# Kernel tuning notes

Hardware: AMD Instinct MI355X
Metric: run time of the kernel (lower is better)

The kernel has to match this reference:

```python
import math
import jax, jax.numpy as jnp
import numpy as np

B, H, W, CV = 8, 64, 64, 256
T, CT = 77, 512
NH, TOP_M = 8, 5
CLAMP = 2.0

def _ln(x, g, b, eps=1e-5):
    mu = x.mean(-1, keepdims=True)
    var = ((x - mu) ** 2).mean(-1, keepdims=True)
    return (x - mu) / jnp.sqrt(var + eps) * g + b

def _l2norm(x, eps=1e-6):
    n = jnp.sqrt((x * x).sum(-1, keepdims=True))
    return x / jnp.maximum(n, eps)

def _xavier(key, fan_in, fan_out):
    a = math.sqrt(6.0 / (fan_in + fan_out))
    return jax.random.uniform(key, (fan_in, fan_out), jnp.float32, -a, a)

def setup_inputs() -> dict:
    key = jax.random.key(0)
    ks = jax.random.split(key, 12)
    inp = {
        'visual_features': jax.random.normal(ks[0], (B, H, W, CV), jnp.float32),
        'text_features': jax.random.normal(ks[1], (B, T, CT), jnp.float32),
        'Wq': _xavier(ks[2], CV, CV), 'bq': jnp.zeros((CV,), jnp.float32),
        'Wk': _xavier(ks[3], CT, CV), 'bk': jnp.zeros((CV,), jnp.float32),
        'Wv': _xavier(ks[4], CT, CV), 'bv': jnp.zeros((CV,), jnp.float32),
        'Wo': _xavier(ks[5], CV, CV), 'bo': jnp.zeros((CV,), jnp.float32),
        'g1': jnp.ones((CV,), jnp.float32), 'b1': jnp.zeros((CV,), jnp.float32),
        'g2': jnp.ones((CV,), jnp.float32), 'b2': jnp.zeros((CV,), jnp.float32),
        'W_ffn1': jax.random.normal(ks[6], (CV, 4 * CV), jnp.float32) * 0.02,
        'b_ffn1': jnp.zeros((4 * CV,), jnp.float32),
        'W_ffn2': jax.random.normal(ks[7], (4 * CV, CV), jnp.float32) * 0.02,
        'b_ffn2': jnp.zeros((CV,), jnp.float32),
        'logit_scale': jnp.float32(math.log(1.0 / 0.07)),
        'alpha': jnp.float32(0.1),
    }
    return inp

def _topm_mask(sim, m):
    # keep only top-m entries along last axis (scatter of top-k indices)
    t = sim.shape[-1]
    _, topi = jax.lax.top_k(sim, m)
    keep = jax.vmap(lambda idx: jnp.zeros((t,), bool).at[idx].set(True))(
        topi.reshape(-1, m)).reshape(sim.shape)
    return jnp.where(keep, sim, -jnp.inf)

def _forward(visual_features, text_features, Wq, bq, Wk, bk, Wv, bv, Wo, bo,
             g1, b1, g2, b2, W_ffn1, b_ffn1, W_ffn2, b_ffn2, logit_scale, alpha):
    b, h, w, cv = visual_features.shape
    n = h * w
    dh = cv // NH
    x = _ln(visual_features, g1, b1).reshape(b, n, cv)      # Pre-LN, (B,N,Cv)
    q = (x @ Wq + bq).reshape(b, n, NH, dh)
    k = (text_features @ Wk + bk).reshape(b, T, NH, dh)
    v = (text_features @ Wv + bv).reshape(b, T, NH, dh)
    q = _l2norm(q); k = _l2norm(k)                           # cosine attention
    scale = jnp.exp(jnp.clip(logit_scale, -CLAMP, CLAMP)) / jnp.sqrt(jnp.float32(dh))
    sim = jnp.einsum('bnhd,bthd->bnht', q, k) * scale        # (B,N,H,T)
    pad = jnp.abs(text_features).sum(-1) <= 1e-6             # (B,T) pad tokens
    sim = jnp.where(pad[:, None, None, :], -jnp.inf, sim)
    sim = _topm_mask(sim, TOP_M)
    attn = jax.nn.softmax(sim, axis=-1)
    all_pad = pad.all(axis=1)                                # (B,)
    attn = jnp.where(all_pad[:, None, None, None], 0.0, attn)
    aligned = jnp.einsum('bnht,bthd->bnhd', attn, v).reshape(b, n, cv)
    aligned = aligned @ Wo + bo
    y = x + alpha * aligned
    y = _ln(y, g2, b2)
    hdn = jax.nn.gelu(y @ W_ffn1 + b_ffn1, approximate=False)
    y = y + (hdn @ W_ffn2 + b_ffn2)
    return y.reshape(b, h, w, cv)

def reference(visual_features, text_features, Wq, bq, Wk, bk, Wv, bv, Wo, bo,
              g1, b1, g2, b2, W_ffn1, b_ffn1, W_ffn2, b_ffn2, logit_scale, alpha):
    return _forward(visual_features, text_features, Wq, bq, Wk, bk, Wv, bv, Wo, bo,
                    g1, b1, g2, b2, W_ffn1, b_ffn1, W_ffn2, b_ffn2, logit_scale, alpha)
```

## Files before the change

kernel.cpp:

```cpp
#include <hip/hip_runtime.h>
#include <math.h>

#define NB   8
#define NPIX 4096
#define MROW 32768
#define CV_  256
#define TT   77
#define CT_  512
#define NH_  8
#define DH_  32
#define BT_  616

typedef __bf16 bf16x8 __attribute__((ext_vector_type(8)));
typedef float  f32x4  __attribute__((ext_vector_type(4)));

__device__ __forceinline__ float bf2f(unsigned short u) {
  return __uint_as_float(((unsigned)u) << 16);
}
__device__ __forceinline__ unsigned short f2b(float f) {
  unsigned u = __float_as_uint(f);
  return (unsigned short)((u + 0x7FFFu + ((u >> 16) & 1u)) >> 16);
}
__device__ __forceinline__ unsigned pack2(float lo, float hi) {
  return ((unsigned)f2b(hi) << 16) | (unsigned)f2b(lo);
}
__device__ __forceinline__ void async_copy16(const unsigned short* g,
                                             unsigned short* l) {
  __builtin_amdgcn_global_load_lds(
      (const __attribute__((address_space(1))) void*)g,
      (__attribute__((address_space(3))) void*)l, 16, 0, 0);
}
__device__ __forceinline__ float gelu_t(float v) {
  float p = v * fmaf(0.0713548162726f, v * v, 1.59576912161f);
  float e = __expf(p);
  return v - v / (e + 1.0f);
}

__global__ __launch_bounds__(256) void prep_kernel(
    const float* __restrict__ visual, const float* __restrict__ g1,
    const float* __restrict__ b1, unsigned short* __restrict__ xbuf,
    const float* __restrict__ s0, const float* __restrict__ s1,
    const float* __restrict__ s2, const float* __restrict__ s3,
    const float* __restrict__ s4, const float* __restrict__ s5,
    unsigned short* __restrict__ d0, unsigned short* __restrict__ d1,
    unsigned short* __restrict__ d2, unsigned short* __restrict__ d3,
    unsigned short* __restrict__ d4, unsigned short* __restrict__ d5,
    const float* __restrict__ bk, const float* __restrict__ bv,
    float* __restrict__ bkv, const float* __restrict__ text,
    float* __restrict__ padb) {
  int bx = blockIdx.x;
  int wave = threadIdx.x >> 6, lane = threadIdx.x & 63;
  if (bx < 8192) {
    int row = bx * 4 + wave;
    size_t base = (size_t)row * 256 + lane * 4;
    float4 f = *reinterpret_cast<const float4*>(visual + base);
    float v0 = f.x, v1 = f.y, v2 = f.z, v3 = f.w;
    float s = v0 + v1 + v2 + v3;
    float q = v0 * v0 + v1 * v1 + v2 * v2 + v3 * v3;
#pragma unroll
    for (int off = 1; off < 64; off <<= 1) {
      s += __shfl_xor(s, off);
      q += __shfl_xor(q, off);
    }
    float mean = s * (1.0f / 256.0f);
    float var  = q * (1.0f / 256.0f) - mean * mean;
    float rstd = rsqrtf(var + 1e-5f);
    float4 gv = *reinterpret_cast<const float4*>(g1 + lane * 4);
    float4 bv4 = *reinterpret_cast<const float4*>(b1 + lane * 4);
    ushort4 o;
    o.x = f2b((v0 - mean) * rstd * gv.x + bv4.x);
    o.y = f2b((v1 - mean) * rstd * gv.y + bv4.y);
    o.z = f2b((v2 - mean) * rstd * gv.z + bv4.z);
    o.w = f2b((v3 - mean) * rstd * gv.w + bv4.w);
    *reinterpret_cast<ushort4*>(xbuf + base) = o;
    return;
  }
  if (bx >= 11778) {
    int row = (bx - 11778) * 4 + wave;
    const float* tr = text + (size_t)row * CT_ + lane * 8;
    float4 f0 = *reinterpret_cast<const float4*>(tr);
    float4 f1 = *reinterpret_cast<const float4*>(tr + 4);
    float s = fabsf(f0.x) + fabsf(f0.y) + fabsf(f0.z) + fabsf(f0.w)
            + fabsf(f1.x) + fabsf(f1.y) + fabsf(f1.z) + fabsf(f1.w);
#pragma unroll
    for (int off = 1; off < 64; off <<= 1) s += __shfl_xor(s, off);
    if (lane == 0) padb[row] = (s <= 1e-6f) ? 1.0f : 0.0f;
    return;
  }
  int gi = (bx - 8192) * 256 + threadIdx.x;
  const float* src; unsigned short* dst; int R, C, idx;
  if      (gi < 65536)  { src=s0; dst=d0; R=256;  C=256;  idx=gi; }
  else if (gi < 196608) { src=s1; dst=d1; R=512;  C=256;  idx=gi-65536; }
  else if (gi < 327680) { src=s2; dst=d2; R=512;  C=256;  idx=gi-196608; }
  else if (gi < 393216) { src=s3; dst=d3; R=256;  C=256;  idx=gi-327680; }
  else if (gi < 655360) { src=s4; dst=d4; R=256;  C=1024; idx=gi-393216; }
  else if (gi < 917504) { src=s5; dst=d5; R=1024; C=256;  idx=gi-655360; }
  else if (gi < 918016) {
    int i = gi - 917504;
    bkv[i] = (i < 256) ? bk[i] : bv[i - 256];
    return;
  } else return;
  int r = idx / C, c = idx - r * C;
  dst[(size_t)c * R + r] = f2b(src[idx]);
}

__global__ __launch_bounds__(256) void qkv_kernel(
    const unsigned short* __restrict__ xb, const unsigned short* __restrict__ WqT,
    const float* __restrict__ bq, unsigned short* __restrict__ qout,
    const float* __restrict__ text, const unsigned short* __restrict__ WkvT,
    const float* __restrict__ bkv, float* __restrict__ kout,
    float* __restrict__ vout) {
  __shared__ unsigned short lA[4096];
  __shared__ unsigned short lB[4096];
  int tid = threadIdx.x;
  int lane = tid & 63, wave = tid >> 6;
  int l15 = lane & 15, quad = lane >> 4;
  if (blockIdx.x < 512) {
    int bm = (blockIdx.x >> 1) * 128, bn = (blockIdx.x & 1) * 128;
    int wm = (wave & 1) * 64, wn = (wave >> 1) * 64;
    int crow = lane >> 2, ccol = (lane & 3) * 8;
    f32x4 acc[4][4] = {};
    for (int k0 = 0; k0 < 256; k0 += 32) {
#pragma unroll
      for (int ch = 0; ch < 2; ++ch) {
        int c = wave * 2 + ch;
        async_copy16(xb + (size_t)(bm + c * 16 + crow) * 256 + k0 + ccol,
                     &lA[c * 512]);
        async_copy16(WqT + (size_t)(bn + c * 16 + crow) * 256 + k0 + ccol,
                     &lB[c * 512]);
      }
      __syncthreads();
      bf16x8 af[4], bfr[4];
#pragma unroll
      for (int mi = 0; mi < 4; ++mi)
        af[mi] = *reinterpret_cast<const bf16x8*>(&lA[(wm + mi * 16 + l15) * 32 + quad * 8]);
#pragma unroll
      for (int ni = 0; ni < 4; ++ni)
        bfr[ni] = *reinterpret_cast<const bf16x8*>(&lB[(wn + ni * 16 + l15) * 32 + quad * 8]);
#pragma unroll
      for (int mi = 0; mi < 4; ++mi)
#pragma unroll
        for (int ni = 0; ni < 4; ++ni)
          acc[mi][ni] = __builtin_amdgcn_mfma_f32_16x16x32_bf16(af[mi], bfr[ni],
                                                                acc[mi][ni], 0, 0, 0);
      __syncthreads();
    }
#pragma unroll
    for (int mi = 0; mi < 4; ++mi) {
#pragma unroll
      for (int ni = 0; ni < 4; ++ni) {
        int gcol = bn + wn + ni * 16 + l15;
        float bsf = bq[gcol];
#pragma unroll
        for (int r = 0; r < 4; ++r) {
          int grow = bm + wm + mi * 16 + quad * 4 + r;
          qout[(size_t)grow * 256 + gcol] = f2b(acc[mi][ni][r] + bsf);
        }
      }
    }
  } else {
    int i = blockIdx.x - 512;
    int bm = (i % 10) * 64, bn = (i / 10) * 64;
    int srow = tid >> 2, sc8 = (tid & 3) * 8;
    int wm = (wave & 1) * 32, wn = (wave >> 1) * 32;
    f32x4 acc[2][2] = {};
    int gm = bm + srow, gn = bn + srow;
    const bool aok = (gm < BT_);
    for (int k0 = 0; k0 < CT_; k0 += 32) {
      uint4 apk = make_uint4(0, 0, 0, 0);
      if (aok) {
        const float* Af = text + (size_t)gm * CT_ + k0 + sc8;
        float4 f0 = *reinterpret_cast<const float4*>(Af);
        float4 f1 = *reinterpret_cast<const float4*>(Af + 4);
        apk.x = pack2(f0.x, f0.y); apk.y = pack2(f0.z, f0.w);
        apk.z = pack2(f1.x, f1.y); apk.w = pack2(f1.z, f1.w);
      }
      uint4 bpk = *reinterpret_cast<const uint4*>(WkvT + (size_t)gn * CT_ + k0 + sc8);
      *reinterpret_cast<uint4*>(&lA[srow * 40 + sc8]) = apk;
      *reinterpret_cast<uint4*>(&lB[srow * 40 + sc8]) = bpk;
      __syncthreads();
      bf16x8 a0 = *reinterpret_cast<const bf16x8*>(&lA[(wm + l15) * 40 + quad * 8]);
      bf16x8 a1 = *reinterpret_cast<const bf16x8*>(&lA[(wm + 16 + l15) * 40 + quad * 8]);
      bf16x8 b0 = *reinterpret_cast<const bf16x8*>(&lB[(wn + l15) * 40 + quad * 8]);
      bf16x8 b1 = *reinterpret_cast<const bf16x8*>(&lB[(wn + 16 + l15) * 40 + quad * 8]);
      acc[0][0] = __builtin_amdgcn_mfma_f32_16x16x32_bf16(a0, b0, acc[0][0], 0, 0, 0);
      acc[0][1] = __builtin_amdgcn_mfma_f32_16x16x32_bf16(a0, b1, acc[0][1], 0, 0, 0);
      acc[1][0] = __builtin_amdgcn_mfma_f32_16x16x32_bf16(a1, b0, acc[1][0], 0, 0, 0);
      acc[1][1] = __builtin_amdgcn_mfma_f32_16x16x32_bf16(a1, b1, acc[1][1], 0, 0, 0);
      __syncthreads();
    }
#pragma unroll
    for (int mt = 0; mt < 2; ++mt) {
#pragma unroll
      for (int nt = 0; nt < 2; ++nt) {
        int gcol = bn + wn + nt * 16 + l15;
        float bsf = bkv[gcol];
#pragma unroll
        for (int r = 0; r < 4; ++r) {
          int grow = bm + wm + mt * 16 + quad * 4 + r;
          if (grow >= BT_) continue;
          float v = acc[mt][nt][r] + bsf;
          if (gcol < 256) kout[(size_t)grow * 256 + gcol] = v;
          else            vout[(size_t)grow * 256 + gcol - 256] = v;
        }
      }
    }
  }
}

__global__ __launch_bounds__(256) void gemm_oln(
    const unsigned short* __restrict__ A, const unsigned short* __restrict__ Bt,
    const float* __restrict__ bias, const unsigned short* __restrict__ xres,
    const float* __restrict__ alpha_ptr,
    const float* __restrict__ g2, const float* __restrict__ b2,
    unsigned short* __restrict__ ybf, float* __restrict__ yf32) {
  __shared__ unsigned short sm[16384];
  unsigned short* lA = sm;
  unsigned short* lB = sm + 2048;
  unsigned short* yt = sm;
  const int K = 256;
  int tid = threadIdx.x;
  int bm = blockIdx.x * 64;
  int lane = tid & 63, wave = tid >> 6;
  int wm = (wave & 1) * 32, wn = (wave >> 1) * 128;
  int l15 = lane & 15, quad = lane >> 4;
  int crow = lane >> 2, ccol = (lane & 3) * 8;
  f32x4 acc[2][8] = {};
  for (int k0 = 0; k0 < K; k0 += 32) {
    async_copy16(A + (size_t)(bm + wave * 16 + crow) * K + k0 + ccol,
                 &lA[wave * 512]);
#pragma unroll
    for (int ch = wave; ch < 16; ch += 4)
      async_copy16(Bt + (size_t)(ch * 16 + crow) * K + k0 + ccol,
                   &lB[ch * 512]);
    __syncthreads();
    bf16x8 af[2], bfr[8];
#pragma unroll
    for (int mi = 0; mi < 2; ++mi)
      af[mi] = *reinterpret_cast<const bf16x8*>(&lA[(wm + mi * 16 + l15) * 32 + quad * 8]);
#pragma unroll
    for (int ni = 0; ni < 8; ++ni)
      bfr[ni] = *reinterpret_cast<const bf16x8*>(&lB[(wn + ni * 16 + l15) * 32 + quad * 8]);
#pragma unroll
    for (int mi = 0; mi < 2; ++mi)
#pragma unroll
      for (int ni = 0; ni < 8; ++ni)
        acc[mi][ni] = __builtin_amdgcn_mfma_f32_16x16x32_bf16(af[mi], bfr[ni],
                                                              acc[mi][ni], 0, 0, 0);
    __syncthreads();
  }
  float alpha = *alpha_ptr;
#pragma unroll
  for (int mi = 0; mi < 2; ++mi) {
#pragma unroll
    for (int ni = 0; ni < 8; ++ni) {
      int gcol = wn + ni * 16 + l15;
      float bsf = bias[gcol];
#pragma unroll
      for (int r = 0; r < 4; ++r) {
        int lrow = wm + mi * 16 + quad * 4 + r;
        float v = acc[mi][ni][r] + bsf;
        float y0 = bf2f(xres[(size_t)(bm + lrow) * 256 + gcol]) + alpha * v;
        yt[lrow * 256 + gcol] = f2b(y0);
      }
    }
  }
  __syncthreads();
  for (int it = 0; it < 16; ++it) {
    int row = wave * 16 + it;
    ushort4 u = *reinterpret_cast<const ushort4*>(&yt[row * 256 + lane * 4]);
    float v0 = bf2f(u.x), v1 = bf2f(u.y), v2 = bf2f(u.z), v3 = bf2f(u.w);
    float s = v0 + v1 + v2 + v3;
    float q = v0 * v0 + v1 * v1 + v2 * v2 + v3 * v3;
#pragma unroll
    for (int off = 1; off < 64; off <<= 1) {
      s += __shfl_xor(s, off);
      q += __shfl_xor(q, off);
    }
    float mean = s * (1.0f / 256.0f);
    float var  = q * (1.0f / 256.0f) - mean * mean;
    float rstd = rsqrtf(var + 1e-5f);
    float4 gv = *reinterpret_cast<const float4*>(g2 + lane * 4);
    float4 bv = *reinterpret_cast<const float4*>(b2 + lane * 4);
    float o0 = (v0 - mean) * rstd * gv.x + bv.x;
    float o1 = (v1 - mean) * rstd * gv.y + bv.y;
    float o2 = (v2 - mean) * rstd * gv.z + bv.z;
    float o3 = (v3 - mean) * rstd * gv.w + bv.w;
    size_t base = (size_t)(bm + row) * 256 + lane * 4;
    ushort4 ob;
    ob.x = f2b(o0); ob.y = f2b(o1); ob.z = f2b(o2); ob.w = f2b(o3);
    *reinterpret_cast<ushort4*>(ybf + base) = ob;
    *reinterpret_cast<float4*>(yf32 + base) = make_float4(o0, o1, o2, o3);
  }
}

#define SSTR 83
#define VSTR 33
#define NEGBIG -3.0e38f
__device__ __forceinline__ void ins5(float sv, float& tv0, float& tv1,
                                     float& tv2, float& tv3, float& tv4) {
  bool g0 = sv > tv0, g1 = sv > tv1, g2 = sv > tv2, g3 = sv > tv3, g4 = sv > tv4;
  tv4 = g4 ? (g3 ? tv3 : sv) : tv4;
  tv3 = g3 ? (g2 ? tv2 : sv) : tv3;
  tv2 = g2 ? (g1 ? tv1 : sv) : tv2;
  tv1 = g1 ? (g0 ? tv0 : sv) : tv1;
  tv0 = g0 ? sv : tv0;
}
__global__ __launch_bounds__(256) void attn_kernel(
    unsigned short* qa, const float* __restrict__ k,
    const float* __restrict__ v, const float* __restrict__ padb,
    const float* __restrict__ ls_ptr) {
  __shared__ unsigned short qb[64 * 40];
  __shared__ unsigned short kb[80 * 40];
  __shared__ float S[64 * SSTR];
  __shared__ float vs[TT * VSTR];
  __shared__ float rn[64];
  __shared__ float scs[80];
  __shared__ int allpad_s;
  int tid = threadIdx.x;
  int h = blockIdx.y, b = blockIdx.z;
  size_t qbase = ((size_t)b * NPIX + blockIdx.x * 64) * CV_ + h * DH_;
  size_t kvbase = (size_t)b * TT * CV_ + h * DH_;
  float ls = *ls_ptr;
  ls = fminf(fmaxf(ls, -2.0f), 2.0f);
  float scale = expf(ls) * 0.17677669529663687f;
  if (tid == 0) allpad_s = 1;
  __syncthreads();
  int qrow = tid >> 2, qq = tid & 3;
  uint4 qv4 = *reinterpret_cast<const uint4*>(qa + qbase + (size_t)qrow * CV_ + qq * 8);
  *reinterpret_cast<uint4*>(&qb[qrow * 40 + qq * 8]) = qv4;
  {
    float ssq = 0.f;
    unsigned w[4] = {qv4.x, qv4.y, qv4.z, qv4.w};
#pragma unroll
    for (int i = 0; i < 4; ++i) {
      float a = bf2f((unsigned short)(w[i] & 0xFFFF));
      float bb = bf2f((unsigned short)(w[i] >> 16));
      ssq += a * a + bb * bb;
    }
    ssq += __shfl_xor(ssq, 1);
    ssq += __shfl_xor(ssq, 2);
    if (qq == 0) rn[qrow] = scale / fmaxf(sqrtf(ssq), 1e-6f);
  }
  if (tid < 154) {
    int kr = tid >> 1, kh = tid & 1;
    const float* kp = k + kvbase + (size_t)kr * CV_ + kh * 16;
    float4 f0 = *reinterpret_cast<const float4*>(kp);
    float4 f1 = *reinterpret_cast<const float4*>(kp + 4);
    float4 f2 = *reinterpret_cast<const float4*>(kp + 8);
    float4 f3 = *reinterpret_cast<const float4*>(kp + 12);
    float ks2 = f0.x*f0.x + f0.y*f0.y + f0.z*f0.z + f0.w*f0.w
              + f1.x*f1.x + f1.y*f1.y + f1.z*f1.z + f1.w*f1.w
              + f2.x*f2.x + f2.y*f2.y + f2.z*f2.z + f2.w*f2.w
              + f3.x*f3.x + f3.y*f3.y + f3.z*f3.z + f3.w*f3.w;
    uint4 p0, p1;
    p0.x = pack2(f0.x, f0.y); p0.y = pack2(f0.z, f0.w);
    p0.z = pack2(f1.x, f1.y); p0.w = pack2(f1.z, f1.w);
    p1.x = pack2(f2.x, f2.y); p1.y = pack2(f2.z, f2.w);
    p1.z = pack2(f3.x, f3.y); p1.w = pack2(f3.z, f3.w);
    *reinterpret_cast<uint4*>(&kb[kr * 40 + kh * 16]) = p0;
    *reinterpret_cast<uint4*>(&kb[kr * 40 + kh * 16 + 8]) = p1;
    ks2 += __shfl_xor(ks2, 1);
    if (kh == 0) {
      float p = padb[b * TT + kr];
      float sc = (p == 0.0f) ? 1.0f / fmaxf(sqrtf(ks2), 1e-6f) : 0.0f;
      scs[kr] = sc;
      if (sc > 0.0f) allpad_s = 0;
    }
  } else if (tid < 157) {
    scs[77 + (tid - 154)] = 0.0f;
  } else if (tid >= 160 && tid < 172) {
    int i = tid - 160;
    *reinterpret_cast<uint4*>(&kb[(77 + (i >> 2)) * 40 + (i & 3) * 8]) =
        make_uint4(0, 0, 0, 0);
  }
  for (int j = tid; j < TT * 8; j += 256) {
    int t = j >> 3, d4 = j & 7;
    float4 f = *reinterpret_cast<const float4*>(
        v + kvbase + (size_t)t * CV_ + d4 * 4);
    float* vp = &vs[t * VSTR + d4 * 4];
    vp[0] = f.x; vp[1] = f.y; vp[2] = f.z; vp[3] = f.w;
  }
  __syncthreads();
  {
    int lane = tid & 63, wave = tid >> 6;
    int wm = wave * 16;
    int l15 = lane & 15, quad = lane >> 4;
    f32x4 acc[5] = {};
    bf16x8 af = *reinterpret_cast<const bf16x8*>(&qb[(wm + l15) * 40 + quad * 8]);
    bf16x8 bfr[5];
#pragma unroll
    for (int ni = 0; ni < 5; ++ni)
      bfr[ni] = *reinterpret_cast<const bf16x8*>(&kb[(ni * 16 + l15) * 40 + quad * 8]);
#pragma unroll
    for (int ni = 0; ni < 5; ++ni)
      acc[ni] = __builtin_amdgcn_mfma_f32_16x16x32_bf16(af, bfr[ni], acc[ni], 0, 0, 0);
#pragma unroll
    for (int ni = 0; ni < 5; ++ni) {
      int col = ni * 16 + l15;
      float sc = scs[col];
#pragma unroll
      for (int r = 0; r < 4; ++r) {
        int row = wm + quad * 4 + r;
        float val = (sc > 0.0f) ? acc[ni][r] * rn[row] * sc : NEGBIG;
        unsigned pb = (__float_as_uint(val) & 0xFFFFFF80u) | (unsigned)col;
        S[row * SSTR + col] = __uint_as_float(pb);
      }
    }
  }
  __syncthreads();
  int allpad = allpad_s;
  int row = qrow;
  const float* Srow = &S[row * SSTR];
  int t0 = qq * 20, t1 = (qq == 3) ? TT : t0 + 20;
  float tv0 = -INFINITY, tv1 = -INFINITY, tv2 = -INFINITY,
        tv3 = -INFINITY, tv4 = -INFINITY;
  for (int t = t0; t < t1; ++t)
    ins5(Srow[t], tv0, tv1, tv2, tv3, tv4);
#pragma unroll
  for (int m = 1; m <= 2; m <<= 1) {
    float n0 = __shfl_xor(tv0, m), n1 = __shfl_xor(tv1, m),
          n2 = __shfl_xor(tv2, m), n3 = __shfl_xor(tv3, m),
          n4 = __shfl_xor(tv4, m);
    ins5(n0, tv0, tv1, tv2, tv3, tv4);
    ins5(n1, tv0, tv1, tv2, tv3, tv4);
    ins5(n2, tv0, tv1, tv2, tv3, tv4);
    ins5(n3, tv0, tv1, tv2, tv3, tv4);
    ins5(n4, tv0, tv1, tv2, tv3, tv4);
  }
  float o[8];
#pragma unroll
  for (int d = 0; d < 8; ++d) o[d] = 0.f;
  if (!allpad) {
    float e0 = 1.0f;
    float e1 = expf(tv1 - tv0);
    float e2 = expf(tv2 - tv0);
    float e3 = expf(tv3 - tv0);
    float e4 = expf(tv4 - tv0);
    float inv = 1.0f / (e0 + e1 + e2 + e3 + e4);
    int i0 = __float_as_uint(tv0) & 0x7F, i1 = __float_as_uint(tv1) & 0x7F,
        i2 = __float_as_uint(tv2) & 0x7F, i3 = __float_as_uint(tv3) & 0x7F,
        i4 = __float_as_uint(tv4) & 0x7F;
    const float* v0p = &vs[i0 * VSTR + qq * 8];
    const float* v1p = &vs[i1 * VSTR + qq * 8];
    const float* v2p = &vs[i2 * VSTR + qq * 8];
    const float* v3p = &vs[i3 * VSTR + qq * 8];
    const float* v4p = &vs[i4 * VSTR + qq * 8];
#pragma unroll
    for (int d = 0; d < 8; ++d)
      o[d] = (e0 * v0p[d] + e1 * v1p[d] + e2 * v2p[d] + e3 * v3p[d] + e4 * v4p[d]) * inv;
  }
  unsigned short* qp = qa + qbase + (size_t)row * CV_ + qq * 8;
  uint4 ou;
  ou.x = ((unsigned)f2b(o[1]) << 16) | f2b(o[0]);
  ou.y = ((unsigned)f2b(o[3]) << 16) | f2b(o[2]);
  ou.z = ((unsigned)f2b(o[5]) << 16) | f2b(o[4]);
  ou.w = ((unsigned)f2b(o[7]) << 16) | f2b(o[6]);
  *reinterpret_cast<uint4*>(qp) = ou;
}

#define XSTR 264
#define HSTR 136
__global__ __launch_bounds__(512) void ffn_fused(
    const unsigned short* __restrict__ ybf, const unsigned short* __restrict__ W1T,
    const float* __restrict__ b1f, const unsigned short* __restrict__ W2T,
    const float* __restrict__ b2f, float* __restrict__ yio) {
  __shared__ unsigned short xs[128 * XSTR];
  __shared__ unsigned short Hs[128 * HSTR];
  __shared__ unsigned short Wb[16384];
  int tid = threadIdx.x, lane = tid & 63, wave = tid >> 6;
  int l15 = lane & 15, quad = lane >> 4;
  int crow = lane >> 2;
  int ccs = (((lane & 3) ^ ((lane >> 3) & 3)) * 8);
  int rsw = ((quad ^ ((l15 >> 1) & 3)) * 8);
  int bm = blockIdx.x * 128;
  {
    int row = tid >> 2, kh = (tid & 3) * 64;
    const unsigned short* src = ybf + (size_t)(bm + row) * 256 + kh;
    unsigned short* dst = &xs[row * XSTR + kh];
#pragma unroll
    for (int i = 0; i < 8; ++i)
      *reinterpret_cast<uint4*>(dst + i * 8) =
          *reinterpret_cast<const uint4*>(src + i * 8);
  }
  int wm2 = (wave & 1) * 64, wn2 = (wave >> 1) * 64;
  int wh1 = (wave & 1) * 64, wr1 = (wave >> 1) * 32;
  auto stage = [&](int st) {
    st &= 63;
    int c = st >> 3, p = st & 7;
    unsigned short* buf = &Wb[(st & 1) * 8192];
    if (p < 4) {
#pragma unroll
      for (int sl = 0; sl < 2; ++sl)
        async_copy16(W1T + (size_t)(c * 128 + wave * 16 + crow) * 256
                         + p * 64 + sl * 32 + ccs,
                     &buf[sl * 4096 + wave * 512]);
    } else {
      int q = p - 4;
#pragma unroll
      for (int i = 0; i < 2; ++i)
        async_copy16(W2T + (size_t)((wave * 2 + i) * 16 + crow) * 1024
                         + c * 128 + q * 32 + ccs,
                     &buf[(wave * 2 + i) * 512]);
    }
  };
  f32x4 acc[4][4] = {};
  stage(0); stage(1);
  for (int c = 0; c < 8; ++c) {
    f32x4 acc1[4][2] = {};
#pragma unroll
    for (int p = 0; p < 8; ++p) {
      int st = c * 8 + p;
      asm volatile("s_waitcnt vmcnt(2) lgkmcnt(0)" ::: "memory");
      __builtin_amdgcn_s_barrier();
      __builtin_amdgcn_sched_barrier(0);
      const unsigned short* buf = &Wb[(p & 1) * 8192];
      if (p < 4) {
#pragma unroll
        for (int sl = 0; sl < 2; ++sl) {
          int k = p * 64 + sl * 32;
          bf16x8 af[4], bfr[2];
#pragma unroll
          for (int mi = 0; mi < 4; ++mi)
            af[mi] = *reinterpret_cast<const bf16x8*>(
                &buf[sl * 4096 + (wh1 + mi * 16 + l15) * 32 + rsw]);
#pragma unroll
          for (int ni = 0; ni < 2; ++ni)
            bfr[ni] = *reinterpret_cast<const bf16x8*>(
                &xs[(wr1 + ni * 16 + l15) * XSTR + k + quad * 8]);
          __builtin_amdgcn_s_setprio(1);
#pragma unroll
          for (int mi = 0; mi < 4; ++mi)
#pragma unroll
            for (int ni = 0; ni < 2; ++ni)
              acc1[mi][ni] = __builtin_amdgcn_mfma_f32_16x16x32_bf16(
                  af[mi], bfr[ni], acc1[mi][ni], 0, 0, 0);
          __builtin_amdgcn_s_setprio(0);
        }
        if (p == 3) {
#pragma unroll
          for (int mi = 0; mi < 4; ++mi) {
            int hb = wh1 + mi * 16 + quad * 4;
            float b0 = b1f[c * 128 + hb],      b1v = b1f[c * 128 + hb + 1];
            float b2v = b1f[c * 128 + hb + 2], b3 = b1f[c * 128 + hb + 3];
#pragma unroll
            for (int ni = 0; ni < 2; ++ni) {
              int row = wr1 + ni * 16 + l15;
              ushort4 hw;
              hw.x = f2b(gelu_t(acc1[mi][ni][0] + b0));
              hw.y = f2b(gelu_t(acc1[mi][ni][1] + b1v));
              hw.z = f2b(gelu_t(acc1[mi][ni][2] + b2v));
              hw.w = f2b(gelu_t(acc1[mi][ni][3] + b3));
              *reinterpret_cast<ushort4*>(&Hs[row * HSTR + hb]) = hw;
            }
          }
        }
      } else {
        int q = p - 4, kk = q * 32;
        bf16x8 af[4], bfr[4];
#pragma unroll
        for (int mi = 0; mi < 4; ++mi)
          af[mi] = *reinterpret_cast<const bf16x8*>(
              &Hs[(wm2 + mi * 16 + l15) * HSTR + kk + quad * 8]);
#pragma unroll
        for (int ni = 0; ni < 4; ++ni)
          bfr[ni] = *reinterpret_cast<const bf16x8*>(
              &buf[(wn2 + ni * 16 + l15) * 32 + rsw]);
        __builtin_amdgcn_s_setprio(1);
#pragma unroll
        for (int mi = 0; mi < 4; ++mi)
#pragma unroll
          for (int ni = 0; ni < 4; ++ni)
            acc[mi][ni] = __builtin_amdgcn_mfma_f32_16x16x32_bf16(
                af[mi], bfr[ni], acc[mi][ni], 0, 0, 0);
        __builtin_amdgcn_s_setprio(0);
      }
      __builtin_amdgcn_sched_barrier(0);
      __builtin_amdgcn_s_barrier();
      __builtin_amdgcn_sched_barrier(0);
      stage(st + 2);
    }
  }
  asm volatile("s_waitcnt vmcnt(0)" ::: "memory");
#pragma unroll
  for (int mi = 0; mi < 4; ++mi)
#pragma unroll
    for (int ni = 0; ni < 4; ++ni) {
      int col = wn2 + ni * 16 + l15;
      float bs = b2f[col];
#pragma unroll
      for (int r = 0; r < 4; ++r) {
        int g = bm + wm2 + mi * 16 + quad * 4 + r;
        size_t oi = (size_t)g * 256 + col;
        yio[oi] = yio[oi] + acc[mi][ni][r] + bs;
      }
    }
}

extern "C" void kernel_launch(void* const* d_in, const int* in_sizes, int n_in,
                              void* d_out, int out_size, void* d_ws, size_t ws_size,
                              hipStream_t stream) {
  const float* visual = (const float*)d_in[0];
  const float* text   = (const float*)d_in[1];
  const float* Wq  = (const float*)d_in[2];
  const float* bq  = (const float*)d_in[3];
  const float* Wk  = (const float*)d_in[4];
  const float* bk  = (const float*)d_in[5];
  const float* Wv  = (const float*)d_in[6];
  const float* bv  = (const float*)d_in[7];
  const float* Wo  = (const float*)d_in[8];
  const float* bo  = (const float*)d_in[9];
  const float* g1  = (const float*)d_in[10];
  const float* b1  = (const float*)d_in[11];
  const float* g2  = (const float*)d_in[12];
  const float* b2  = (const float*)d_in[13];
  const float* W1  = (const float*)d_in[14];
  const float* bf1 = (const float*)d_in[15];
  const float* W2  = (const float*)d_in[16];
  const float* bff2 = (const float*)d_in[17];
  const float* lsc = (const float*)d_in[18];
  const float* alp = (const float*)d_in[19];

  char* ws = (char*)d_ws;
  size_t off = 0;
  auto alloc = [&](size_t bytes) -> char* {
    char* p = ws + off;
    off += (bytes + 255) & ~(size_t)255;
    return p;
  };
  unsigned short* WqT = (unsigned short*)alloc((size_t)65536 * 2);
  unsigned short* WkT = (unsigned short*)alloc((size_t)131072 * 2);
  unsigned short* WvT = (unsigned short*)alloc((size_t)131072 * 2);
  unsigned short* WoT = (unsigned short*)alloc((size_t)65536 * 2);
  unsigned short* W1T = (unsigned short*)alloc((size_t)262144 * 2);
  unsigned short* W2T = (unsigned short*)alloc((size_t)262144 * 2);
  float*          bkv  = (float*)alloc(512 * 4);
  float*          kbuf = (float*)alloc((size_t)BT_ * CV_ * 4);
  float*          vbuf = (float*)alloc((size_t)BT_ * CV_ * 4);
  float*          padb = (float*)alloc((size_t)BT_ * 4);
  char* U = ws + off;
  unsigned short* xbuf = (unsigned short*)U;
  unsigned short* qbuf = (unsigned short*)(U + 16777216);
  float*          ybuf = (float*)d_out;

  prep_kernel<<<11932, 256, 0, stream>>>(visual, g1, b1, xbuf,
                                         Wq, Wk, Wv, Wo, W1, W2,
                                         WqT, WkT, WvT, WoT, W1T, W2T,
                                         bk, bv, bkv, text, padb);
  qkv_kernel<<<592, 256, 0, stream>>>(xbuf, WqT, bq, qbuf,
                                      text, WkT, bkv, kbuf, vbuf);
  attn_kernel<<<dim3(64, NH_, NB), 256, 0, stream>>>(qbuf, kbuf, vbuf, padb, lsc);
  gemm_oln<<<512, 256, 0, stream>>>(qbuf, WoT, bo, xbuf, alp, g2, b2,
                                    xbuf, ybuf);
  ffn_fused<<<256, 512, 0, stream>>>(xbuf, W1T, bf1, W2T, bff2, ybuf);
}
```

Measured before the change: 287.2 us.

## Triple-buffer FFN weight stages, drop bf16 y copy, cache bias in LDS

The FFN kernel's weight staging goes from two buffers to three. This lets the next prefetch be issued right after the single top-of-iteration barrier, so the second barrier per step can be removed. The LN2 output epilogue no longer writes a separate bf16 copy; the FFN kernel instead reads the fp32 y and converts it to bf16 while filling LDS. The FFN1 bias is also loaded once into LDS and read there as float4. In exchange, the kernel uses more LDS (possible occupancy loss) and reads twice as many bytes for the input tile.

```diff
diff --git a/kernel.cpp b/kernel.cpp
--- a/kernel.cpp
+++ b/kernel.cpp
@@ -213,7 +213,7 @@
     const float* __restrict__ bias, const unsigned short* __restrict__ xres,
     const float* __restrict__ alpha_ptr,
     const float* __restrict__ g2, const float* __restrict__ b2,
-    unsigned short* __restrict__ ybf, float* __restrict__ yf32) {
+    float* __restrict__ yf32) {
   __shared__ unsigned short sm[16384];
   unsigned short* lA = sm;
   unsigned short* lB = sm + 2048;
@@ -287,9 +287,6 @@
     float o2 = (v2 - mean) * rstd * gv.z + bv.z;
     float o3 = (v3 - mean) * rstd * gv.w + bv.w;
     size_t base = (size_t)(bm + row) * 256 + lane * 4;
-    ushort4 ob;
-    ob.x = f2b(o0); ob.y = f2b(o1); ob.z = f2b(o2); ob.w = f2b(o3);
-    *reinterpret_cast<ushort4*>(ybf + base) = ob;
     *reinterpret_cast<float4*>(yf32 + base) = make_float4(o0, o1, o2, o3);
   }
 }
@@ -462,33 +459,42 @@
 #define XSTR 264
 #define HSTR 136
 __global__ __launch_bounds__(512) void ffn_fused(
-    const unsigned short* __restrict__ ybf, const unsigned short* __restrict__ W1T,
+    const float* yin, const unsigned short* __restrict__ W1T,
     const float* __restrict__ b1f, const unsigned short* __restrict__ W2T,
-    const float* __restrict__ b2f, float* __restrict__ yio) {
+    const float* __restrict__ b2f, float* yio) {
   __shared__ unsigned short xs[128 * XSTR];
   __shared__ unsigned short Hs[128 * HSTR];
-  __shared__ unsigned short Wb[16384];
+  __shared__ unsigned short Wb[24576];
+  __shared__ float bls[1024];
   int tid = threadIdx.x, lane = tid & 63, wave = tid >> 6;
   int l15 = lane & 15, quad = lane >> 4;
   int crow = lane >> 2;
   int ccs = (((lane & 3) ^ ((lane >> 3) & 3)) * 8);
   int rsw = ((quad ^ ((l15 >> 1) & 3)) * 8);
   int bm = blockIdx.x * 128;
+  if (tid < 256) {
+    float4 bb = *reinterpret_cast<const float4*>(b1f + tid * 4);
+    *reinterpret_cast<float4*>(&bls[tid * 4]) = bb;
+  }
   {
     int row = tid >> 2, kh = (tid & 3) * 64;
-    const unsigned short* src = ybf + (size_t)(bm + row) * 256 + kh;
+    const float* src = yin + (size_t)(bm + row) * 256 + kh;
     unsigned short* dst = &xs[row * XSTR + kh];
 #pragma unroll
-    for (int i = 0; i < 8; ++i)
-      *reinterpret_cast<uint4*>(dst + i * 8) =
-          *reinterpret_cast<const uint4*>(src + i * 8);
+    for (int i = 0; i < 8; ++i) {
+      float4 f0 = *reinterpret_cast<const float4*>(src + i * 8);
+      float4 f1 = *reinterpret_cast<const float4*>(src + i * 8 + 4);
+      uint4 u;
+      u.x = pack2(f0.x, f0.y); u.y = pack2(f0.z, f0.w);
+      u.z = pack2(f1.x, f1.y); u.w = pack2(f1.z, f1.w);
+      *reinterpret_cast<uint4*>(dst + i * 8) = u;
+    }
   }
   int wm2 = (wave & 1) * 64, wn2 = (wave >> 1) * 64;
   int wh1 = (wave & 1) * 64, wr1 = (wave >> 1) * 32;
-  auto stage = [&](int st) {
-    st &= 63;
-    int c = st >> 3, p = st & 7;
-    unsigned short* buf = &Wb[(st & 1) * 8192];
+  auto stage = [&](int cs, int bsel) {
+    int c = cs >> 3, p = cs & 7;
+    unsigned short* buf = &Wb[bsel * 8192];
     if (p < 4) {
 #pragma unroll
       for (int sl = 0; sl < 2; ++sl)
@@ -505,7 +511,8 @@
     }
   };
   f32x4 acc[4][4] = {};
-  stage(0); stage(1);
+  stage(0, 0); stage(1, 1);
+  int wsel = 2, rsel = 0;
   for (int c = 0; c < 8; ++c) {
     f32x4 acc1[4][2] = {};
 #pragma unroll
@@ -514,7 +521,10 @@
       asm volatile("s_waitcnt vmcnt(2) lgkmcnt(0)" ::: "memory");
       __builtin_amdgcn_s_barrier();
       __builtin_amdgcn_sched_barrier(0);
-      const unsigned short* buf = &Wb[(p & 1) * 8192];
+      stage((st + 2) & 63, wsel);
+      wsel = (wsel == 2) ? 0 : wsel + 1;
+      const unsigned short* buf = &Wb[rsel * 8192];
+      rsel = (rsel == 2) ? 0 : rsel + 1;
       if (p < 4) {
 #pragma unroll
         for (int sl = 0; sl < 2; ++sl) {
@@ -541,16 +551,15 @@
 #pragma unroll
           for (int mi = 0; mi < 4; ++mi) {
             int hb = wh1 + mi * 16 + quad * 4;
-            float b0 = b1f[c * 128 + hb],      b1v = b1f[c * 128 + hb + 1];
-            float b2v = b1f[c * 128 + hb + 2], b3 = b1f[c * 128 + hb + 3];
+            float4 bb = *reinterpret_cast<const float4*>(&bls[c * 128 + hb]);
 #pragma unroll
             for (int ni = 0; ni < 2; ++ni) {
               int row = wr1 + ni * 16 + l15;
               ushort4 hw;
-              hw.x = f2b(gelu_t(acc1[mi][ni][0] + b0));
-              hw.y = f2b(gelu_t(acc1[mi][ni][1] + b1v));
-              hw.z = f2b(gelu_t(acc1[mi][ni][2] + b2v));
-              hw.w = f2b(gelu_t(acc1[mi][ni][3] + b3));
+              hw.x = f2b(gelu_t(acc1[mi][ni][0] + bb.x));
+              hw.y = f2b(gelu_t(acc1[mi][ni][1] + bb.y));
+              hw.z = f2b(gelu_t(acc1[mi][ni][2] + bb.z));
+              hw.w = f2b(gelu_t(acc1[mi][ni][3] + bb.w));
               *reinterpret_cast<ushort4*>(&Hs[row * HSTR + hb]) = hw;
             }
           }
@@ -575,10 +584,6 @@
                 af[mi], bfr[ni], acc[mi][ni], 0, 0, 0);
         __builtin_amdgcn_s_setprio(0);
       }
-      __builtin_amdgcn_sched_barrier(0);
-      __builtin_amdgcn_s_barrier();
-      __builtin_amdgcn_sched_barrier(0);
-      stage(st + 2);
     }
   }
   asm volatile("s_waitcnt vmcnt(0)" ::: "memory");
@@ -650,7 +655,6 @@
   qkv_kernel<<<592, 256, 0, stream>>>(xbuf, WqT, bq, qbuf,
                                       text, WkT, bkv, kbuf, vbuf);
   attn_kernel<<<dim3(64, NH_, NB), 256, 0, stream>>>(qbuf, kbuf, vbuf, padb, lsc);
-  gemm_oln<<<512, 256, 0, stream>>>(qbuf, WoT, bo, xbuf, alp, g2, b2,
-                                    xbuf, ybuf);
-  ffn_fused<<<256, 512, 0, stream>>>(xbuf, W1T, bf1, W2T, bff2, ybuf);
-}
+  gemm_oln<<<512, 256, 0, stream>>>(qbuf, WoT, bo, xbuf, alp, g2, b2, ybuf);
+  ffn_fused<<<256, 512, 0, stream>>>(ybuf, W1T, bf1, W2T, bff2, ybuf);
+}
```

After: 296.6 us. 3.3% more time.
